# Kernel tuning notes

Measured on AMD Instinct MI355X. Metric: run time of the kernel, lower is better.

Reference implementation:

```python
import jax, jax.numpy as jnp
import numpy as np

ETA = 0.01
EPSILON = 1e-08


def setup_inputs() -> dict:
    key = jax.random.key(0)
    k1, k2 = jax.random.split(key)
    B, N = 2000000, 16  # batch (time steps), num_assets
    weights = jax.random.uniform(k1, (B, N), dtype=jnp.float32)
    next_returns = jax.random.normal(k2, (B, N), dtype=jnp.float32) * 0.02
    return {"weights": weights, "next_returns": next_returns}


def reference(weights, next_returns):
    # portfolio return per time step: (B,)
    R = jnp.sum(weights * next_returns, axis=1)
    batch_size = R.shape[0]
    eta = jnp.asarray(ETA, R.dtype)
    eps = jnp.asarray(EPSILON, R.dtype)

    def step(carry, R_t):
        A_prev, B_prev = carry
        delta_A = eta * (R_t - A_prev)
        delta_B = eta * (R_t * R_t - B_prev)
        variance = jnp.maximum(B_prev - A_prev * A_prev, eps)
        denom = variance ** 1.5
        D_t = (B_prev * delta_A - 0.5 * A_prev * delta_B) / denom
        return (A_prev + delta_A, B_prev + delta_B), D_t

    init = (jnp.asarray(0.0, R.dtype), jnp.asarray(EPSILON, R.dtype))
    _, D = jax.lax.scan(step, init, R)
    return -jnp.sum(D) / batch_size
```

## Files before the change

kernel.cpp:

```cpp
#include <hip/hip_runtime.h>


#define D_ETA 0.01
#define D_C   (1.0 - D_ETA)
#define D_EPS 1e-8

constexpr int BLOCK  = 256;
constexpr int CHUNK  = 1024;
constexpr int LPT    = CHUNK / BLOCK;
constexpr int PASSES = CHUNK / 64;

typedef float f32x4 __attribute__((ext_vector_type(4)));

__device__ __forceinline__ void block_scan(double& m, double& sA, double& sB,
                                           double* mS, double* aS, double* bS) {
    int tid = threadIdx.x;
    mS[tid] = m; aS[tid] = sA; bS[tid] = sB;
    __syncthreads();
#pragma unroll
    for (int off = 1; off < BLOCK; off <<= 1) {
        double pm = 1.0, pa = 0.0, pb = 0.0;
        if (tid >= off) { pm = mS[tid - off]; pa = aS[tid - off]; pb = bS[tid - off]; }
        __syncthreads();
        if (tid >= off) {
            sA = m * pa + sA;
            sB = m * pb + sB;
            m  = pm * m;
        }
        mS[tid] = m; aS[tid] = sA; bS[tid] = sB;
        __syncthreads();
    }
}

__global__ __launch_bounds__(BLOCK, 4) void k1_fused(
    const float* __restrict__ w, const float* __restrict__ x, int nrows,
    float* __restrict__ Rws,
    double* __restrict__ blkM, double* __restrict__ blkA, double* __restrict__ blkB)
{
    __shared__ double Qs[4][CHUNK];
    __shared__ double mS[BLOCK], aS[BLOCK], bS[BLOCK];

    const int tid = threadIdx.x;
    const int b   = blockIdx.x;
    const long long base = (long long)b * CHUNK;
    const int q    = tid & 3;
    const int rsub = tid >> 2;
    const f32x4* w4 = (const f32x4*)w;
    const f32x4* x4 = (const f32x4*)x;

    const bool full = (base + CHUNK <= (long long)nrows);

    if (full) {
        const long long f0 = base * 4 + tid;
        f32x4 a0 = __builtin_nontemporal_load(&w4[f0]);
        f32x4 c0 = __builtin_nontemporal_load(&x4[f0]);
        f32x4 a1 = __builtin_nontemporal_load(&w4[f0 + 256]);
        f32x4 c1 = __builtin_nontemporal_load(&x4[f0 + 256]);
        f32x4 a2 = __builtin_nontemporal_load(&w4[f0 + 512]);
        f32x4 c2 = __builtin_nontemporal_load(&x4[f0 + 512]);
#pragma unroll
        for (int p = 0; p < PASSES; ++p) {
            f32x4 a3 = (f32x4)(0.f);
            f32x4 c3 = (f32x4)(0.f);
            if (p + 3 < PASSES) {
                a3 = __builtin_nontemporal_load(&w4[f0 + (long long)(p + 3) * 256]);
                c3 = __builtin_nontemporal_load(&x4[f0 + (long long)(p + 3) * 256]);
            }
            __builtin_amdgcn_sched_barrier(0);
            double d = (double)a0.x * c0.x + (double)a0.y * c0.y
                     + (double)a0.z * c0.z + (double)a0.w * c0.w;
            Qs[q][p * 64 + rsub] = d;
            a0 = a1; c0 = c1;
            a1 = a2; c1 = c2;
            a2 = a3; c2 = c3;
        }
    } else {
        for (int p = 0; p < PASSES; ++p) {
            long long row = base + (long long)p * 64 + rsub;
            if (row < (long long)nrows) {
                long long f = row * 4 + q;
                f32x4 a = w4[f], c = x4[f];
                Qs[q][p * 64 + rsub] =
                      (double)a.x * c.x + (double)a.y * c.y
                    + (double)a.z * c.z + (double)a.w * c.w;
            }
        }
    }
    __syncthreads();

    long long g0 = base + (long long)tid * LPT;
    long long rem = (long long)nrows - g0;
    int len = rem >= LPT ? LPT : (rem > 0 ? (int)rem : 0);

    float rv[LPT];
#pragma unroll
    for (int r = 0; r < LPT; ++r) {
        int lr = tid * LPT + r;
        double d01 = Qs[0][lr] + Qs[1][lr];
        double d23 = Qs[2][lr] + Qs[3][lr];
        rv[r] = (float)(d01 + d23);
    }

    if (len == LPT) {
        *(float4*)(Rws + g0) = make_float4(rv[0], rv[1], rv[2], rv[3]);
    } else {
        for (int k = 0; k < len; ++k) Rws[g0 + k] = rv[k];
    }

    double m = 1.0, sA = 0.0, sB = 0.0;
    for (int k = 0; k < len; ++k) {
        double r = (double)rv[k];
        sA = D_C * sA + D_ETA * r;
        sB = D_C * sB + D_ETA * (r * r);
        m *= D_C;
    }
    block_scan(m, sA, sB, mS, aS, bS);
    if (tid == BLOCK - 1) {
        blkM[b] = m;
        blkA[b] = sA;
        blkB[b] = sB;
    }
}

__device__ __forceinline__ float row_R(const float* __restrict__ w,
                                       const float* __restrict__ x,
                                       long long row) {
    const float4* w4 = (const float4*)(w + row * 16);
    const float4* x4 = (const float4*)(x + row * 16);
    double d0 = 0.0, d1 = 0.0, d2 = 0.0, d3 = 0.0;
    {
        float4 a = w4[0], b = x4[0];
        d0 = (double)a.x * b.x + (double)a.y * b.y
           + (double)a.z * b.z + (double)a.w * b.w;
    }
    {
        float4 a = w4[1], b = x4[1];
        d1 = (double)a.x * b.x + (double)a.y * b.y
           + (double)a.z * b.z + (double)a.w * b.w;
    }
    {
        float4 a = w4[2], b = x4[2];
        d2 = (double)a.x * b.x + (double)a.y * b.y
           + (double)a.z * b.z + (double)a.w * b.w;
    }
    {
        float4 a = w4[3], b = x4[3];
        d3 = (double)a.x * b.x + (double)a.y * b.y
           + (double)a.z * b.z + (double)a.w * b.w;
    }
    return (float)((d0 + d1) + (d2 + d3));
}

__device__ __forceinline__ int load_seg(const float* __restrict__ Rws,
                                        const float* __restrict__ w,
                                        const float* __restrict__ x,
                                        long long g0, int nrows, float* rv) {
    long long rem = (long long)nrows - g0;
    int len = rem >= LPT ? LPT : (rem > 0 ? (int)rem : 0);
    if (Rws) {
        if (len == LPT) {
            float4 u = *(const float4*)(Rws + g0);
            rv[0] = u.x; rv[1] = u.y; rv[2] = u.z; rv[3] = u.w;
        } else {
            for (int k = 0; k < len; ++k) rv[k] = Rws[g0 + k];
        }
    } else {
        for (int k = 0; k < len; ++k) rv[k] = row_R(w, x, g0 + k);
    }
    return len;
}

__global__ __launch_bounds__(BLOCK) void k2_partials(
    const float* __restrict__ Rws,
    const float* __restrict__ w, const float* __restrict__ x, int nrows,
    double* __restrict__ blkM, double* __restrict__ blkA, double* __restrict__ blkB)
{
    __shared__ double mS[BLOCK], aS[BLOCK], bS[BLOCK];
    int tid = threadIdx.x;
    long long g0 = (long long)blockIdx.x * CHUNK + (long long)tid * LPT;
    float rv[LPT];
    int len = load_seg(Rws, w, x, g0, nrows, rv);

    double m = 1.0, sA = 0.0, sB = 0.0;
    for (int k = 0; k < len; ++k) {
        double r = (double)rv[k];
        sA = D_C * sA + D_ETA * r;
        sB = D_C * sB + D_ETA * (r * r);
        m *= D_C;
    }
    block_scan(m, sA, sB, mS, aS, bS);
    if (tid == BLOCK - 1) {
        blkM[blockIdx.x] = m;
        blkA[blockIdx.x] = sA;
        blkB[blockIdx.x] = sB;
    }
}

__global__ __launch_bounds__(BLOCK) void k3_scan(
    int nb,
    const double* __restrict__ blkM, const double* __restrict__ blkA,
    const double* __restrict__ blkB,
    double* __restrict__ A0, double* __restrict__ B0)
{
    __shared__ double mS[BLOCK], aS[BLOCK], bS[BLOCK];
    int tid = threadIdx.x;
    int K = (nb + BLOCK - 1) / BLOCK;
    int g0 = tid * K;
    int g1 = g0 + K; if (g1 > nb) g1 = nb;

    double m = 1.0, sA = 0.0, sB = 0.0;
    for (int g = g0; g < g1; ++g) {
        double mg = blkM[g], ag = blkA[g], bg = blkB[g];
        sA = mg * sA + ag;
        sB = mg * sB + bg;
        m *= mg;
    }
    block_scan(m, sA, sB, mS, aS, bS);

    double em = 1.0, ea = 0.0, eb = 0.0;
    if (tid > 0) { em = mS[tid - 1]; ea = aS[tid - 1]; eb = bS[tid - 1]; }
    double A = ea;
    double B = em * D_EPS + eb;
    for (int g = g0; g < g1; ++g) {
        A0[g] = A; B0[g] = B;
        double mg = blkM[g], ag = blkA[g], bg = blkB[g];
        A = mg * A + ag;
        B = mg * B + bg;
    }
}

__global__ __launch_bounds__(BLOCK) void k4_dsum(
    const float* __restrict__ Rws,
    const float* __restrict__ w, const float* __restrict__ x, int nrows,
    const double* __restrict__ A0, const double* __restrict__ B0,
    double* __restrict__ bsum)
{
    __shared__ double mS[BLOCK], aS[BLOCK], bS[BLOCK];
    __shared__ double wsum[BLOCK / 64];
    int tid = threadIdx.x;
    long long g0 = (long long)blockIdx.x * CHUNK + (long long)tid * LPT;
    float rv[LPT];
    int len = load_seg(Rws, w, x, g0, nrows, rv);

    double m = 1.0, sA = 0.0, sB = 0.0;
    for (int k = 0; k < len; ++k) {
        double r = (double)rv[k];
        sA = D_C * sA + D_ETA * r;
        sB = D_C * sB + D_ETA * (r * r);
        m *= D_C;
    }
    block_scan(m, sA, sB, mS, aS, bS);

    double em = 1.0, ea = 0.0, eb = 0.0;
    if (tid > 0) { em = mS[tid - 1]; ea = aS[tid - 1]; eb = bS[tid - 1]; }
    double A = em * A0[blockIdx.x] + ea;
    double B = em * B0[blockIdx.x] + eb;

    double dsum = 0.0;
    for (int k = 0; k < len; ++k) {
        double r = (double)rv[k];
        double dA = D_ETA * (r - A);
        double dB = D_ETA * (r * r - B);
        double var = B - A * A;
        if (var < D_EPS) var = D_EPS;
        double denom = var * sqrt(var);
        dsum += (B * dA - 0.5 * A * dB) / denom;
        A += dA;
        B += dB;
    }

#pragma unroll
    for (int off = 32; off > 0; off >>= 1) dsum += __shfl_down(dsum, off, 64);
    if ((tid & 63) == 0) wsum[tid >> 6] = dsum;
    __syncthreads();
    if (tid == 0) bsum[blockIdx.x] = wsum[0] + wsum[1] + wsum[2] + wsum[3];
}

__global__ __launch_bounds__(BLOCK) void k5_final(
    const double* __restrict__ bsum, int nb, int nrows, float* __restrict__ out)
{
    __shared__ double sh[BLOCK / 64];
    int tid = threadIdx.x;
    double s = 0.0;
    for (int i = tid; i < nb; i += BLOCK) s += bsum[i];
#pragma unroll
    for (int off = 32; off > 0; off >>= 1) s += __shfl_down(s, off, 64);
    if ((tid & 63) == 0) sh[tid >> 6] = s;
    __syncthreads();
    if (tid == 0) out[0] = (float)(-(sh[0] + sh[1] + sh[2] + sh[3]) / (double)nrows);
}

extern "C" void kernel_launch(void* const* d_in, const int* in_sizes, int n_in,
                              void* d_out, int out_size, void* d_ws, size_t ws_size,
                              hipStream_t stream)
{
    const float* w = (const float*)d_in[0];
    const float* x = (const float*)d_in[1];
    int nrows = in_sizes[0] / 16;
    int nb  = (nrows + CHUNK - 1) / CHUNK;

    char* ws = (char*)d_ws;
    double* blkM = (double*)(ws + 64);
    double* blkA = blkM + nb;
    double* blkB = blkA + nb;
    double* A0   = blkB + nb;
    double* B0   = A0 + nb;
    double* bsum = B0 + nb;

    size_t off = 64 + (size_t)6 * nb * sizeof(double);
    off = (off + 255) & ~(size_t)255;
    float* Rws = nullptr;
    if (ws_size >= off + (size_t)nrows * sizeof(float))
        Rws = (float*)(ws + off);

    if (Rws) {
        k1_fused<<<nb, BLOCK, 0, stream>>>(w, x, nrows, Rws, blkM, blkA, blkB);
    } else {
        k2_partials<<<nb, BLOCK, 0, stream>>>(Rws, w, x, nrows, blkM, blkA, blkB);
    }
    k3_scan<<<1, BLOCK, 0, stream>>>(nb, blkM, blkA, blkB, A0, B0);
    k4_dsum<<<nb, BLOCK, 0, stream>>>(Rws, w, x, nrows, A0, B0, bsum);
    k5_final<<<1, BLOCK, 0, stream>>>(bsum, nb, nrows, (float*)d_out);
}
```

Baseline: 267.8 us.

## Halve k1 shared staging via lane shuffle, deepen prefetch, raise occupancy hint

In the fused first kernel, adjacent lanes now combine their partial dot products with a lane shuffle, so only half the lanes write to shared memory and the staging array shrinks from four to two slices. The load pipeline is one stage deeper (four in flight instead of three), and the launch bound asks for six blocks per SM instead of four. The Rws reload in the second pass now uses a nontemporal load. Together these aim to lower LDS footprint and traffic and hide more memory latency, at the cost of more live registers for prefetch, which may conflict with the higher occupancy target.

Result: no change. 267.5 us (-0.1%).

```diff
diff --git a/kernel.cpp b/kernel.cpp
--- a/kernel.cpp
+++ b/kernel.cpp
@@ -32,12 +32,12 @@
     }
 }
 
-__global__ __launch_bounds__(BLOCK, 4) void k1_fused(
+__global__ __launch_bounds__(BLOCK, 6) void k1_fused(
     const float* __restrict__ w, const float* __restrict__ x, int nrows,
     float* __restrict__ Rws,
     double* __restrict__ blkM, double* __restrict__ blkA, double* __restrict__ blkB)
 {
-    __shared__ double Qs[4][CHUNK];
+    __shared__ double Qs[2][CHUNK];
     __shared__ double mS[BLOCK], aS[BLOCK], bS[BLOCK];
 
     const int tid = threadIdx.x;
@@ -58,32 +58,40 @@
         f32x4 c1 = __builtin_nontemporal_load(&x4[f0 + 256]);
         f32x4 a2 = __builtin_nontemporal_load(&w4[f0 + 512]);
         f32x4 c2 = __builtin_nontemporal_load(&x4[f0 + 512]);
+        f32x4 a3 = __builtin_nontemporal_load(&w4[f0 + 768]);
+        f32x4 c3 = __builtin_nontemporal_load(&x4[f0 + 768]);
 #pragma unroll
         for (int p = 0; p < PASSES; ++p) {
-            f32x4 a3 = (f32x4)(0.f);
-            f32x4 c3 = (f32x4)(0.f);
-            if (p + 3 < PASSES) {
-                a3 = __builtin_nontemporal_load(&w4[f0 + (long long)(p + 3) * 256]);
-                c3 = __builtin_nontemporal_load(&x4[f0 + (long long)(p + 3) * 256]);
+            f32x4 an = (f32x4)(0.f);
+            f32x4 cn = (f32x4)(0.f);
+            if (p + 4 < PASSES) {
+                an = __builtin_nontemporal_load(&w4[f0 + (long long)(p + 4) * 256]);
+                cn = __builtin_nontemporal_load(&x4[f0 + (long long)(p + 4) * 256]);
             }
             __builtin_amdgcn_sched_barrier(0);
             double d = (double)a0.x * c0.x + (double)a0.y * c0.y
                      + (double)a0.z * c0.z + (double)a0.w * c0.w;
-            Qs[q][p * 64 + rsub] = d;
+            d += __shfl_xor(d, 1, 64);
+            if ((q & 1) == 0)
+                Qs[q >> 1][p * 64 + rsub] = d;
             a0 = a1; c0 = c1;
             a1 = a2; c1 = c2;
             a2 = a3; c2 = c3;
+            a3 = an; c3 = cn;
         }
     } else {
         for (int p = 0; p < PASSES; ++p) {
             long long row = base + (long long)p * 64 + rsub;
+            double d = 0.0;
             if (row < (long long)nrows) {
                 long long f = row * 4 + q;
                 f32x4 a = w4[f], c = x4[f];
-                Qs[q][p * 64 + rsub] =
-                      (double)a.x * c.x + (double)a.y * c.y
-                    + (double)a.z * c.z + (double)a.w * c.w;
+                d = (double)a.x * c.x + (double)a.y * c.y
+                  + (double)a.z * c.z + (double)a.w * c.w;
             }
+            d += __shfl_xor(d, 1, 64);
+            if ((q & 1) == 0 && row < (long long)nrows)
+                Qs[q >> 1][p * 64 + rsub] = d;
         }
     }
     __syncthreads();
@@ -96,9 +104,7 @@
 #pragma unroll
     for (int r = 0; r < LPT; ++r) {
         int lr = tid * LPT + r;
-        double d01 = Qs[0][lr] + Qs[1][lr];
-        double d23 = Qs[2][lr] + Qs[3][lr];
-        rv[r] = (float)(d01 + d23);
+        rv[r] = (float)(Qs[0][lr] + Qs[1][lr]);
     }
 
     if (len == LPT) {
@@ -127,7 +133,7 @@
                                        long long row) {
     const float4* w4 = (const float4*)(w + row * 16);
     const float4* x4 = (const float4*)(x + row * 16);
-    double d0 = 0.0, d1 = 0.0, d2 = 0.0, d3 = 0.0;
+    double d0, d1, d2, d3;
     {
         float4 a = w4[0], b = x4[0];
         d0 = (double)a.x * b.x + (double)a.y * b.y
@@ -159,7 +165,7 @@
     int len = rem >= LPT ? LPT : (rem > 0 ? (int)rem : 0);
     if (Rws) {
         if (len == LPT) {
-            float4 u = *(const float4*)(Rws + g0);
+            f32x4 u = __builtin_nontemporal_load((const f32x4*)(Rws + g0));
             rv[0] = u.x; rv[1] = u.y; rv[2] = u.z; rv[3] = u.w;
         } else {
             for (int k = 0; k < len; ++k) rv[k] = Rws[g0 + k];
```
